# Optimization experiments

Hardware: AMD Instinct MI355X
Metric: run time of the kernel (lower is better)

## Reference

```python
import jax, jax.numpy as jnp
import numpy as np

D_MODEL = 2048
N_HEADS = 4
IDX_DIM = 64
B, TQ, TK = 2, 4096, 4096


def setup_inputs() -> dict:
    key = jax.random.key(0)
    k1, k2, k3, k4, k5 = jax.random.split(key, 5)
    x_q = jax.random.normal(k1, (B, TQ, D_MODEL), dtype=jnp.float32)
    x_k = jax.random.normal(k2, (B, TK, D_MODEL), dtype=jnp.float32)
    scale = 1.0 / np.sqrt(D_MODEL)
    Wq = jax.random.normal(k3, (D_MODEL, N_HEADS * IDX_DIM), dtype=jnp.float32) * scale
    Ww = jax.random.normal(k4, (D_MODEL, N_HEADS), dtype=jnp.float32) * scale
    Wk = jax.random.normal(k5, (D_MODEL, IDX_DIM), dtype=jnp.float32) * scale
    return {"x_q": x_q, "x_k": x_k, "Wq": Wq, "Ww": Ww, "Wk": Wk}


def reference(x_q, x_k, Wq, Ww, Wk):
    Bq, Tq, _ = x_q.shape
    # q_I: (B, Tq, H, d_idx); w_I: (B, Tq, H); k_I: (B, Tk, d_idx)
    q_I = (x_q @ Wq).reshape(Bq, Tq, N_HEADS, IDX_DIM)
    w_I = x_q @ Ww
    k_I = x_k @ Wk
    # per-head dot scores: (B, H, Tq, Tk), key projection shared across heads
    dot = jnp.einsum("bqhd,bkd->bhqk", q_I, k_I)
    activated = jax.nn.relu(dot)
    # weighted sum over heads -> (B, Tq, Tk)
    index_scores = jnp.einsum("bhqk,bqh->bqk", activated, w_I)
    return index_scores
```

## Files before the change

kernel.cpp:

```cpp
#include <hip/hip_runtime.h>
#include <hip/hip_bf16.h>

#define DM 2048
#define NH 4
#define DI 64
#define TQS 4096
#define TKS 4096
#define BB 2

typedef __attribute__((ext_vector_type(4))) float f32x4;
typedef __attribute__((ext_vector_type(8))) short bf16x8;

__device__ __forceinline__ short f2bf(float f) {
  __hip_bfloat16 h = __float2bfloat16(f);
  return __builtin_bit_cast(short, h);
}

__device__ __forceinline__ bf16x8 cvt8(f32x4 a, f32x4 b) {
  bf16x8 r;
  r[0] = f2bf(a[0]); r[1] = f2bf(a[1]); r[2] = f2bf(a[2]); r[3] = f2bf(a[3]);
  r[4] = f2bf(b[0]); r[5] = f2bf(b[1]); r[6] = f2bf(b[2]); r[7] = f2bf(b[3]);
  return r;
}

__global__ __launch_bounds__(256) void transpose_qw(const float* __restrict__ Wq,
                                                    const float* __restrict__ Ww,
                                                    short* __restrict__ WT) {
  int idx = blockIdx.x * 256 + threadIdx.x;
  int n = idx >> 11, k = idx & 2047;
  float v = 0.f;
  if (n < 256) v = Wq[(size_t)k * 256 + n];
  else if (n < 260) v = Ww[(size_t)k * 4 + (n - 256)];
  WT[idx] = f2bf(v);
}

__global__ __launch_bounds__(256) void transpose_k(const float* __restrict__ Wk,
                                                   short* __restrict__ WT) {
  int idx = blockIdx.x * 256 + threadIdx.x;
  int n = idx >> 11, k = idx & 2047;
  WT[idx] = f2bf(Wk[(size_t)k * 64 + n]);
}

template <int NJ, bool QP>
__device__ __forceinline__ void proj_body(const float* __restrict__ X,
                                          const short* __restrict__ WT,
                                          short* __restrict__ O,
                                          float* __restrict__ wI, int blk) {
  const int tid = threadIdx.x;
  const int wave = tid >> 6, lane = tid & 63;
  const int l15 = lane & 15, quad = lane >> 4;
  const int m0 = blk * 32;
  const int ldo = QP ? 256 : 64;

  int jt[NJ];
#pragma unroll
  for (int jj = 0; jj < NJ; ++jj) jt[jj] = QP ? (jj < 4 ? jj * 4 + wave : 16 + wave) : wave;

  const float* xbase = X + (size_t)(m0 + l15) * DM + quad * 8;
  const short* wb[NJ];
#pragma unroll
  for (int jj = 0; jj < NJ; ++jj) wb[jj] = WT + (size_t)(jt[jj] * 16 + l15) * DM + quad * 8;

  const f32x4 z = {0.f, 0.f, 0.f, 0.f};
  f32x4 acc[NJ][2];
#pragma unroll
  for (int jj = 0; jj < NJ; ++jj)
#pragma unroll
    for (int i = 0; i < 2; ++i) acc[jj][i] = z;

  f32x4 araw[4][2][2];
  bf16x8 bb[4][NJ];
#pragma unroll
  for (int s = 0; s < 4; ++s) {
#pragma unroll
    for (int i = 0; i < 2; ++i) {
      araw[s][i][0] = *(const f32x4*)(xbase + s * 32 + i * 16 * DM);
      araw[s][i][1] = *(const f32x4*)(xbase + s * 32 + i * 16 * DM + 4);
    }
#pragma unroll
    for (int jj = 0; jj < NJ; ++jj) bb[s][jj] = *(const bf16x8*)(wb[jj] + s * 32);
  }

#pragma unroll 4
  for (int ks = 0; ks < 64; ++ks) {
    const int s = ks & 3;
    bf16x8 abf[2];
#pragma unroll
    for (int i = 0; i < 2; ++i) abf[i] = cvt8(araw[s][i][0], araw[s][i][1]);
    if (ks < 60) {
      const float* xp = xbase + (ks + 4) * 32;
#pragma unroll
      for (int i = 0; i < 2; ++i) {
        araw[s][i][0] = *(const f32x4*)(xp + i * 16 * DM);
        araw[s][i][1] = *(const f32x4*)(xp + i * 16 * DM + 4);
      }
    }
#pragma unroll
    for (int jj = 0; jj < NJ; ++jj)
#pragma unroll
      for (int i = 0; i < 2; ++i)
        acc[jj][i] = __builtin_amdgcn_mfma_f32_16x16x32_bf16(abf[i], bb[s][jj],
                                                             acc[jj][i], 0, 0, 0);
    if (ks < 60) {
#pragma unroll
      for (int jj = 0; jj < NJ; ++jj)
        bb[s][jj] = *(const bf16x8*)(wb[jj] + (ks + 4) * 32);
    }
  }

#pragma unroll
  for (int jj = 0; jj < NJ; ++jj) {
    if (QP && jt[jj] >= 16) {
      if (jt[jj] == 16 && l15 < 4) {
#pragma unroll
        for (int i = 0; i < 2; ++i)
#pragma unroll
          for (int r = 0; r < 4; ++r)
            wI[(size_t)(m0 + i * 16 + quad * 4 + r) * NH + l15] = acc[jj][i][r];
      }
    } else {
#pragma unroll
      for (int i = 0; i < 2; ++i)
#pragma unroll
        for (int r = 0; r < 4; ++r)
          O[(size_t)(m0 + i * 16 + quad * 4 + r) * ldo + jt[jj] * 16 + l15] =
              f2bf(acc[jj][i][r]);
    }
  }
}

__global__ __launch_bounds__(256, 2) void proj_fused(const float* __restrict__ xq,
                                                     const float* __restrict__ xk,
                                                     const short* __restrict__ WqwT,
                                                     const short* __restrict__ WkT,
                                                     short* __restrict__ qb,
                                                     short* __restrict__ kb,
                                                     float* __restrict__ wIb) {
  if (blockIdx.x < 256)
    proj_body<5, true>(xq, WqwT, qb, wIb, blockIdx.x);
  else
    proj_body<1, false>(xk, WkT, kb, nullptr, blockIdx.x - 256);
}

__global__ __launch_bounds__(256, 2) void score_kernel(const short* __restrict__ qb,
                                                       const short* __restrict__ kb,
                                                       const float* __restrict__ wI,
                                                       float* __restrict__ out) {
  const int b = blockIdx.z;
  const int qt = blockIdx.y;
  const int kt = blockIdx.x;
  const int tid = threadIdx.x;
  const int wave = tid >> 6, lane = tid & 63;
  const int wm = wave >> 1, wn = wave & 1;
  const int l15 = lane & 15, quad = lane >> 4;

  bf16x8 bf[4][2];
  {
    const short* kbase =
        kb + (size_t)(b * TKS + kt * 128 + wn * 64 + l15) * DI + quad * 8;
#pragma unroll
    for (int j = 0; j < 4; ++j)
#pragma unroll
      for (int ks = 0; ks < 2; ++ks)
        bf[j][ks] = *(const bf16x8*)(kbase + j * 16 * DI + ks * 32);
  }

  const f32x4 z = {0.f, 0.f, 0.f, 0.f};
  f32x4 facc[4][4];
#pragma unroll
  for (int i = 0; i < 4; ++i)
#pragma unroll
    for (int j = 0; j < 4; ++j) facc[i][j] = z;

  const short* qbase =
      qb + (size_t)(b * TQS + qt * 128 + wm * 64 + l15) * (NH * DI) + quad * 8;
  const float* wbase = wI + (size_t)(b * TQS + qt * 128 + wm * 64 + quad * 4) * NH;

  bf16x8 af[2][4][2];
#pragma unroll
  for (int i = 0; i < 4; ++i)
#pragma unroll
    for (int ks = 0; ks < 2; ++ks)
      af[0][i][ks] = *(const bf16x8*)(qbase + i * 16 * (NH * DI) + ks * 32);

#pragma unroll
  for (int h = 0; h < NH; ++h) {
    if (h < NH - 1) {
#pragma unroll
      for (int i = 0; i < 4; ++i)
#pragma unroll
        for (int ks = 0; ks < 2; ++ks)
          af[(h + 1) & 1][i][ks] =
              *(const bf16x8*)(qbase + (h + 1) * DI + i * 16 * (NH * DI) + ks * 32);
    }

    f32x4 acc[4][4];
#pragma unroll
    for (int i = 0; i < 4; ++i)
#pragma unroll
      for (int j = 0; j < 4; ++j) acc[i][j] = z;

#pragma unroll
    for (int ks = 0; ks < 2; ++ks)
#pragma unroll
      for (int i = 0; i < 4; ++i)
#pragma unroll
        for (int j = 0; j < 4; ++j)
          acc[i][j] = __builtin_amdgcn_mfma_f32_16x16x32_bf16(
              af[h & 1][i][ks], bf[j][ks], acc[i][j], 0, 0, 0);

#pragma unroll
    for (int i = 0; i < 4; ++i) {
      float wv[4];
#pragma unroll
      for (int r = 0; r < 4; ++r) wv[r] = wbase[(i * 16 + r) * NH + h];
#pragma unroll
      for (int j = 0; j < 4; ++j)
#pragma unroll
        for (int r = 0; r < 4; ++r)
          facc[i][j][r] += wv[r] * fmaxf(acc[i][j][r], 0.f);
    }
  }

  float* obase = out + (size_t)b * TQS * TKS +
                 (size_t)(qt * 128 + wm * 64 + quad * 4) * TKS + kt * 128 + wn * 64 + l15;
#pragma unroll
  for (int i = 0; i < 4; ++i)
#pragma unroll
    for (int r = 0; r < 4; ++r)
#pragma unroll
      for (int j = 0; j < 4; ++j)
        __builtin_nontemporal_store(facc[i][j][r],
                                    &obase[(size_t)(i * 16 + r) * TKS + j * 16]);
}

extern "C" void kernel_launch(void* const* d_in, const int* in_sizes, int n_in,
                              void* d_out, int out_size, void* d_ws, size_t ws_size,
                              hipStream_t stream) {
  const float* x_q = (const float*)d_in[0];
  const float* x_k = (const float*)d_in[1];
  const float* Wq  = (const float*)d_in[2];
  const float* Ww  = (const float*)d_in[3];
  const float* Wk  = (const float*)d_in[4];
  float* out = (float*)d_out;

  char* ws = (char*)d_ws;
  short* qbuf = (short*)(ws);
  short* kbuf = (short*)(ws + (4u << 20));
  float* wIb  = (float*)(ws + (5u << 20));
  short* WqwT = (short*)(ws + (5u << 20) + (128u << 10));
  short* WkT  = (short*)(ws + (7u << 20));

  transpose_qw<<<(320 * 2048) / 256, 256, 0, stream>>>(Wq, Ww, WqwT);
  transpose_k<<<(64 * 2048) / 256, 256, 0, stream>>>(Wk, WkT);

  proj_fused<<<512, 256, 0, stream>>>(x_q, x_k, WqwT, WkT, qbuf, kbuf, wIb);

  score_kernel<<<dim3(TKS / 128, TQS / 128, BB), 256, 0, stream>>>(qbuf, kbuf, wIb, out);
}
```

Baseline: 355.2 us.

## Stage projection X tiles through double-buffered LDS via direct global-to-LDS loads

The projection kernel now loads each 32x64 fp32 tile of X straight into a double-buffered shared-memory array using global_load_lds, with an XOR swizzle to avoid bank conflicts. Each wave reads its MFMA operands from LDS instead of every wave reloading the same rows from global memory into registers. This cuts redundant global traffic and register pressure across the four waves. In exchange it adds a barrier per k-step and a shallower prefetch depth than the previous four-stage register pipeline. The weight operands are still loaded from global memory each iteration.

```diff
diff --git a/kernel.cpp b/kernel.cpp
--- a/kernel.cpp
+++ b/kernel.cpp
@@ -10,6 +10,9 @@
 
 typedef __attribute__((ext_vector_type(4))) float f32x4;
 typedef __attribute__((ext_vector_type(8))) short bf16x8;
+
+typedef __attribute__((address_space(1))) const void gvoid;
+typedef __attribute__((address_space(3))) void lvoid;
 
 __device__ __forceinline__ short f2bf(float f) {
   __hip_bfloat16 h = __float2bfloat16(f);
@@ -45,7 +48,8 @@
 __device__ __forceinline__ void proj_body(const float* __restrict__ X,
                                           const short* __restrict__ WT,
                                           short* __restrict__ O,
-                                          float* __restrict__ wI, int blk) {
+                                          float* __restrict__ wI, int blk,
+                                          float* As ) {
   const int tid = threadIdx.x;
   const int wave = tid >> 6, lane = tid & 63;
   const int l15 = lane & 15, quad = lane >> 4;
@@ -56,10 +60,16 @@
 #pragma unroll
   for (int jj = 0; jj < NJ; ++jj) jt[jj] = QP ? (jj < 4 ? jj * 4 + wave : 16 + wave) : wave;
 
-  const float* xbase = X + (size_t)(m0 + l15) * DM + quad * 8;
   const short* wb[NJ];
 #pragma unroll
   for (int jj = 0; jj < NJ; ++jj) wb[jj] = WT + (size_t)(jt[jj] * 16 + l15) * DM + quad * 8;
+
+  const int srow = tid >> 4;
+  const int schunk = (tid & 15) ^ srow;
+  const float* s0 = X + (size_t)(m0 + srow) * DM + schunk * 4;
+  const float* s1 = X + (size_t)(m0 + 16 + srow) * DM + schunk * 4;
+  const int d0 = tid * 16;
+  const int d1 = 4096 + tid * 16;
 
   const f32x4 z = {0.f, 0.f, 0.f, 0.f};
   f32x4 acc[NJ][2];
@@ -68,44 +78,56 @@
 #pragma unroll
     for (int i = 0; i < 2; ++i) acc[jj][i] = z;
 
-  f32x4 araw[4][2][2];
-  bf16x8 bb[4][NJ];
-#pragma unroll
-  for (int s = 0; s < 4; ++s) {
-#pragma unroll
-    for (int i = 0; i < 2; ++i) {
-      araw[s][i][0] = *(const f32x4*)(xbase + s * 32 + i * 16 * DM);
-      araw[s][i][1] = *(const f32x4*)(xbase + s * 32 + i * 16 * DM + 4);
-    }
-#pragma unroll
-    for (int jj = 0; jj < NJ; ++jj) bb[s][jj] = *(const bf16x8*)(wb[jj] + s * 32);
-  }
-
-#pragma unroll 4
-  for (int ks = 0; ks < 64; ++ks) {
-    const int s = ks & 3;
-    bf16x8 abf[2];
-#pragma unroll
-    for (int i = 0; i < 2; ++i) abf[i] = cvt8(araw[s][i][0], araw[s][i][1]);
-    if (ks < 60) {
-      const float* xp = xbase + (ks + 4) * 32;
-#pragma unroll
-      for (int i = 0; i < 2; ++i) {
-        araw[s][i][0] = *(const f32x4*)(xp + i * 16 * DM);
-        araw[s][i][1] = *(const f32x4*)(xp + i * 16 * DM + 4);
+  char* lbase = (char*)As;
+
+  __builtin_amdgcn_global_load_lds((gvoid*)s0, (lvoid*)(lbase + d0), 16, 0, 0);
+  __builtin_amdgcn_global_load_lds((gvoid*)s1, (lvoid*)(lbase + d1), 16, 0, 0);
+  __syncthreads();
+
+  int cur = 0;
+#pragma unroll 2
+  for (int t = 0; t < 32; ++t) {
+    bf16x8 bbv[NJ][2];
+#pragma unroll
+    for (int jj = 0; jj < NJ; ++jj)
+#pragma unroll
+      for (int ks = 0; ks < 2; ++ks)
+        bbv[jj][ks] = *(const bf16x8*)(wb[jj] + t * 64 + ks * 32);
+    __builtin_amdgcn_sched_barrier(0);
+
+    if (t < 31) {
+      const float* g0 = s0 + (t + 1) * 64;
+      const float* g1 = s1 + (t + 1) * 64;
+      char* l = lbase + (cur ^ 1) * 8192;
+      __builtin_amdgcn_global_load_lds((gvoid*)g0, (lvoid*)(l + d0), 16, 0, 0);
+      __builtin_amdgcn_global_load_lds((gvoid*)g1, (lvoid*)(l + d1), 16, 0, 0);
+    }
+    __builtin_amdgcn_sched_barrier(0);
+
+    const float* Ab = As + cur * 2048;
+    bf16x8 abf[2][2];
+#pragma unroll
+    for (int i = 0; i < 2; ++i)
+#pragma unroll
+      for (int ks = 0; ks < 2; ++ks) {
+        const int rb = (i * 16 + l15) * 64;
+        const int cg = ks * 8 + quad * 2;
+        f32x4 a0 = *(const f32x4*)(Ab + rb + ((cg ^ l15) << 2));
+        f32x4 a1 = *(const f32x4*)(Ab + rb + (((cg + 1) ^ l15) << 2));
+        abf[i][ks] = cvt8(a0, a1);
       }
-    }
+
 #pragma unroll
     for (int jj = 0; jj < NJ; ++jj)
 #pragma unroll
       for (int i = 0; i < 2; ++i)
-        acc[jj][i] = __builtin_amdgcn_mfma_f32_16x16x32_bf16(abf[i], bb[s][jj],
-                                                             acc[jj][i], 0, 0, 0);
-    if (ks < 60) {
-#pragma unroll
-      for (int jj = 0; jj < NJ; ++jj)
-        bb[s][jj] = *(const bf16x8*)(wb[jj] + (ks + 4) * 32);
-    }
+#pragma unroll
+        for (int ks = 0; ks < 2; ++ks)
+          acc[jj][i] = __builtin_amdgcn_mfma_f32_16x16x32_bf16(abf[i][ks], bbv[jj][ks],
+                                                               acc[jj][i], 0, 0, 0);
+
+    __syncthreads();
+    cur ^= 1;
   }
 
 #pragma unroll
@@ -136,10 +158,11 @@
                                                      short* __restrict__ qb,
                                                      short* __restrict__ kb,
                                                      float* __restrict__ wIb) {
+  __shared__ __align__(16) float As[2][2048];
   if (blockIdx.x < 256)
-    proj_body<5, true>(xq, WqwT, qb, wIb, blockIdx.x);
+    proj_body<5, true>(xq, WqwT, qb, wIb, blockIdx.x, &As[0][0]);
   else
-    proj_body<1, false>(xk, WkT, kb, nullptr, blockIdx.x - 256);
+    proj_body<1, false>(xk, WkT, kb, nullptr, blockIdx.x - 256, &As[0][0]);
 }
 
 __global__ __launch_bounds__(256, 2) void score_kernel(const short* __restrict__ qb,
```

Result: faster. 301.6 us (-15.1%).
